# Kernel tuning notes

Measured on AMD Instinct MI355X. Metric: run time of the kernel, lower is better.

Reference implementation:

```python
import jax, jax.numpy as jnp
import numpy as np

# Hardcoded grouping buffer from GroupedPNMLP (6 groups x 4 nodes, permutation of 0..23)
GROUPING = np.array([[0, 3, 6, 9], [1, 4, 7, 10], [2, 5, 8, 11],
                     [12, 13, 14, 15], [16, 18, 20, 22], [17, 19, 21, 23]], dtype=np.int32)
INV_PERM = np.argsort(GROUPING.reshape(-1))  # scatter back to node order

N_SAMPLES = 131072
N_NODES = 24
IN_CH = 32
HID = 32
OUT_CH = 1
N_GROUPS = 6
NODES_PER_GROUP = 4


def setup_inputs() -> dict:
    key = jax.random.key(0)
    k = jax.random.split(key, 5)
    h = jax.random.normal(k[0], (N_SAMPLES, N_NODES, IN_CH), dtype=jnp.float32)
    valid = jax.random.randint(k[1], (N_SAMPLES, N_NODES), 0, 2).astype(jnp.int32)
    # Stacked ParallelLinear weights across the 6 group networks (D=2: in->W, W->out)
    W1 = jax.random.normal(k[2], (N_GROUPS, NODES_PER_GROUP, IN_CH, HID), dtype=jnp.float32) * 0.1
    b1 = jnp.zeros((N_GROUPS, NODES_PER_GROUP, HID), dtype=jnp.float32)
    W2 = jax.random.normal(k[3], (N_GROUPS, NODES_PER_GROUP, HID, OUT_CH), dtype=jnp.float32) * 0.1
    b2 = jnp.zeros((N_GROUPS, NODES_PER_GROUP, OUT_CH), dtype=jnp.float32)
    return {"h": h, "valid": valid, "W1": W1, "b1": b1, "W2": W2, "b2": b2}


def reference(h, valid, W1, b1, W2, b2):
    # Gather per-group node features: [N, 6, 4, 32]
    hg = h[:, GROUPING]
    # input_relu=True -> ReLU on input, then ParallelLinear -> ReLU -> ParallelLinear
    x = jnp.maximum(hg, 0.0)
    x = jnp.einsum('bgkl,gklj->bgkj', x, W1) + b1  # [N, 6, 4, 32]
    x = jnp.maximum(x, 0.0)
    out = jnp.einsum('bgkl,gklj->bgkj', x, W2) + b2  # [N, 6, 4, 1]
    # Samples whose group has no valid node are left as zeros (matches torch.where gather)
    group_valid = (valid[:, GROUPING].sum(-1) > 0)  # [N, 6]
    out = out * group_valid[:, :, None, None].astype(out.dtype)
    flat = out.reshape(out.shape[0], N_NODES, OUT_CH)
    # scatter_ with grouping indices == inverse permutation back to node order
    return flat[:, INV_PERM]
```

## Files before the change

kernel.cpp:

```cpp
#include <hip/hip_runtime.h>

#define N_NODES 24
#define CH 32

__global__ __launch_bounds__(256) void grouped_pnmlp_kernel(
    const float* __restrict__ h,
    const int*   __restrict__ valid,
    const float* __restrict__ W1,
    const float* __restrict__ b1,
    const float* __restrict__ W2,
    const float* __restrict__ b2,
    float*       __restrict__ out,
    int n_samples)
{
    const int node = blockIdx.y;

    int g, k;
    if (node < 12)      { g = node % 3;               k = node / 3;        }
    else if (node < 16) { g = 3;                      k = node - 12;       }
    else                { g = 4 + ((node - 16) & 1);  k = (node - 16) >> 1; }

    int vbase, vstride;
    if (g < 3)       { vbase = g;            vstride = 3; }
    else if (g == 3) { vbase = 12;           vstride = 1; }
    else             { vbase = 16 + (g - 4); vstride = 2; }

    const int gk = g * 4 + k;
    const float* __restrict__ w1  = W1 + (size_t)gk * CH * CH;
    const float* __restrict__ w2  = W2 + (size_t)gk * CH;
    const float* __restrict__ bb1 = b1 + (size_t)gk * CH;
    const float               bb2 = b2[gk];

    const int b = blockIdx.x * blockDim.x + threadIdx.x;
    if (b >= n_samples) return;

    const float4* __restrict__ xp =
        (const float4*)(h + ((size_t)b * N_NODES + node) * CH);
    float x[CH];
#pragma unroll
    for (int i = 0; i < 8; ++i) {
        float4 v = xp[i];
        x[4*i+0] = fmaxf(v.x, 0.0f);
        x[4*i+1] = fmaxf(v.y, 0.0f);
        x[4*i+2] = fmaxf(v.z, 0.0f);
        x[4*i+3] = fmaxf(v.w, 0.0f);
    }

    float hid[CH];
#pragma unroll
    for (int j = 0; j < CH; ++j) hid[j] = bb1[j];
#pragma unroll
    for (int l = 0; l < CH; ++l) {
        const float xl = x[l];
#pragma unroll
        for (int j = 0; j < CH; ++j)
            hid[j] = fmaf(xl, w1[l * CH + j], hid[j]);
    }

    float acc = bb2;
#pragma unroll
    for (int j = 0; j < CH; ++j)
        acc = fmaf(fmaxf(hid[j], 0.0f), w2[j], acc);

    const int* __restrict__ vrow = valid + (size_t)b * N_NODES;
    const int vs = vrow[vbase] + vrow[vbase + vstride] +
                   vrow[vbase + 2 * vstride] + vrow[vbase + 3 * vstride];

    out[(size_t)b * N_NODES + node] = (vs > 0) ? acc : 0.0f;
}

extern "C" void kernel_launch(void* const* d_in, const int* in_sizes, int n_in,
                              void* d_out, int out_size, void* d_ws, size_t ws_size,
                              hipStream_t stream) {
    const float* h     = (const float*)d_in[0];
    const int*   valid = (const int*)d_in[1];
    const float* W1    = (const float*)d_in[2];
    const float* b1    = (const float*)d_in[3];
    const float* W2    = (const float*)d_in[4];
    const float* b2    = (const float*)d_in[5];
    float* out = (float*)d_out;

    const int n_samples = in_sizes[0] / (N_NODES * CH);

    dim3 block(256, 1, 1);
    dim3 grid((n_samples + 255) / 256, N_NODES, 1);
    grouped_pnmlp_kernel<<<grid, block, 0, stream>>>(h, valid, W1, b1, W2, b2,
                                                     out, n_samples);
}
```

Baseline: 608.3 us.

## Stage contiguous node features in LDS with coalesced loads, one wave per node

Each block now covers 64 samples and 6 consecutive nodes. It loads the whole contiguous 6-node slab of h cooperatively as coalesced float4 reads into shared memory, applying the ReLU during the load. Each wave then handles one node, so the weight address is wave-uniform, and lanes read their sample's features from LDS instead of strided global loads. The validity masks are computed once per sample from vectorized int4 loads, and outputs are written out coalesced through shared memory. This adds two block barriers and about 50KB of LDS per block, which limits occupancy.

```diff
diff --git a/kernel.cpp b/kernel.cpp
--- a/kernel.cpp
+++ b/kernel.cpp
@@ -2,8 +2,11 @@
 
 #define N_NODES 24
 #define CH 32
+#define SPB 64
+#define NPQ 6
+#define THREADS 384
 
-__global__ __launch_bounds__(256) void grouped_pnmlp_kernel(
+__global__ __launch_bounds__(THREADS) void grouped_pnmlp_kernel(
     const float* __restrict__ h,
     const int*   __restrict__ valid,
     const float* __restrict__ W1,
@@ -13,17 +16,54 @@
     float*       __restrict__ out,
     int n_samples)
 {
-    const int node = blockIdx.y;
+    __shared__ float xs[SPB][196];
+    __shared__ float gs[SPB][6];
+    __shared__ float os[SPB][NPQ];
+
+    const int t  = threadIdx.x;
+    const int q  = blockIdx.y;
+    const int s0 = blockIdx.x * SPB;
+
+    const float4* __restrict__ hv = (const float4*)h;
+    float4 r[8];
+#pragma unroll
+    for (int i = 0; i < 8; ++i) {
+        const int f = i * THREADS + t;
+        const int s = f / 48, c = f % 48;
+        int sg = s0 + s; if (sg >= n_samples) sg = n_samples - 1;
+        r[i] = hv[(size_t)sg * 192 + q * 48 + c];
+    }
+#pragma unroll
+    for (int i = 0; i < 8; ++i) {
+        const int f = i * THREADS + t;
+        const int s = f / 48, c = f % 48;
+        float4 v = r[i];
+        v.x = fmaxf(v.x, 0.0f); v.y = fmaxf(v.y, 0.0f);
+        v.z = fmaxf(v.z, 0.0f); v.w = fmaxf(v.w, 0.0f);
+        *(float4*)&xs[s][4 * c] = v;
+    }
+
+    if (t < SPB) {
+        int sg = s0 + t; if (sg >= n_samples) sg = n_samples - 1;
+        const int4* __restrict__ vp = (const int4*)(valid + (size_t)sg * N_NODES);
+        const int4 a = vp[0], b = vp[1], c = vp[2], d = vp[3], e = vp[4], f = vp[5];
+        gs[t][0] = (a.x + a.w + b.z + c.y > 0) ? 1.0f : 0.0f;
+        gs[t][1] = (a.y + b.x + b.w + c.z > 0) ? 1.0f : 0.0f;
+        gs[t][2] = (a.z + b.y + c.x + c.w > 0) ? 1.0f : 0.0f;
+        gs[t][3] = (d.x + d.y + d.z + d.w > 0) ? 1.0f : 0.0f;
+        gs[t][4] = (e.x + e.z + f.x + f.z > 0) ? 1.0f : 0.0f;
+        gs[t][5] = (e.y + e.w + f.y + f.w > 0) ? 1.0f : 0.0f;
+    }
+    __syncthreads();
+
+    const int w    = __builtin_amdgcn_readfirstlane(t >> 6);
+    const int lane = t & 63;
+    const int node = q * NPQ + w;
 
     int g, k;
     if (node < 12)      { g = node % 3;               k = node / 3;        }
     else if (node < 16) { g = 3;                      k = node - 12;       }
     else                { g = 4 + ((node - 16) & 1);  k = (node - 16) >> 1; }
-
-    int vbase, vstride;
-    if (g < 3)       { vbase = g;            vstride = 3; }
-    else if (g == 3) { vbase = 12;           vstride = 1; }
-    else             { vbase = 16 + (g - 4); vstride = 2; }
 
     const int gk = g * 4 + k;
     const float* __restrict__ w1  = W1 + (size_t)gk * CH * CH;
@@ -31,19 +71,11 @@
     const float* __restrict__ bb1 = b1 + (size_t)gk * CH;
     const float               bb2 = b2[gk];
 
-    const int b = blockIdx.x * blockDim.x + threadIdx.x;
-    if (b >= n_samples) return;
-
-    const float4* __restrict__ xp =
-        (const float4*)(h + ((size_t)b * N_NODES + node) * CH);
     float x[CH];
 #pragma unroll
     for (int i = 0; i < 8; ++i) {
-        float4 v = xp[i];
-        x[4*i+0] = fmaxf(v.x, 0.0f);
-        x[4*i+1] = fmaxf(v.y, 0.0f);
-        x[4*i+2] = fmaxf(v.z, 0.0f);
-        x[4*i+3] = fmaxf(v.w, 0.0f);
+        const float4 v = *(const float4*)&xs[lane][w * CH + 4 * i];
+        x[4*i+0] = v.x; x[4*i+1] = v.y; x[4*i+2] = v.z; x[4*i+3] = v.w;
     }
 
     float hid[CH];
@@ -62,11 +94,15 @@
     for (int j = 0; j < CH; ++j)
         acc = fmaf(fmaxf(hid[j], 0.0f), w2[j], acc);
 
-    const int* __restrict__ vrow = valid + (size_t)b * N_NODES;
-    const int vs = vrow[vbase] + vrow[vbase + vstride] +
-                   vrow[vbase + 2 * vstride] + vrow[vbase + 3 * vstride];
+    os[lane][w] = acc * gs[lane][g];
+    __syncthreads();
 
-    out[(size_t)b * N_NODES + node] = (vs > 0) ? acc : 0.0f;
+    {
+        const int s = t / 6, j = t % 6;
+        const int sg = s0 + s;
+        if (sg < n_samples)
+            out[(size_t)sg * N_NODES + q * NPQ + j] = os[s][j];
+    }
 }
 
 extern "C" void kernel_launch(void* const* d_in, const int* in_sizes, int n_in,
@@ -82,8 +118,8 @@
 
     const int n_samples = in_sizes[0] / (N_NODES * CH);
 
-    dim3 block(256, 1, 1);
-    dim3 grid((n_samples + 255) / 256, N_NODES, 1);
+    dim3 block(THREADS, 1, 1);
+    dim3 grid((n_samples + SPB - 1) / SPB, 4, 1);
     grouped_pnmlp_kernel<<<grid, block, 0, stream>>>(h, valid, W1, b1, W2, b2,
                                                      out, n_samples);
 }
```

Measured after the change: 611.5 us. No clear change (+0.5%).

## Process 64 samples per block with waves looping over nodes and prefetching

Applied to the files above, without the earlier changes.

Replaces the per-node grid dimension with blocks of 64 samples, where each of 4 waves handles 6 nodes in turn, keeping the node index wave-uniform. The valid row is loaded once per sample as int4 vectors and all six group masks are computed up front, instead of four scalar loads per node. The next node's 128-byte feature row is prefetched into registers while the current node computes. This raises register pressure (cur and nxt buffers alongside the 32-wide hidden vector) and may lower occupancy. Weight reads stay wave-uniform, so they can still come from scalar loads.

```diff
diff --git a/kernel.cpp b/kernel.cpp
--- a/kernel.cpp
+++ b/kernel.cpp
@@ -2,8 +2,12 @@
 
 #define N_NODES 24
 #define CH 32
+#define SPW 64
+#define WAVES 4
+#define THREADS 256
+#define NPW 6
 
-__global__ __launch_bounds__(256) void grouped_pnmlp_kernel(
+__global__ __launch_bounds__(THREADS) void grouped_pnmlp_kernel(
     const float* __restrict__ h,
     const int*   __restrict__ valid,
     const float* __restrict__ W1,
@@ -13,60 +17,83 @@
     float*       __restrict__ out,
     int n_samples)
 {
-    const int node = blockIdx.y;
+    const int w    = __builtin_amdgcn_readfirstlane(threadIdx.x >> 6);
+    const int lane = threadIdx.x & 63;
 
-    int g, k;
-    if (node < 12)      { g = node % 3;               k = node / 3;        }
-    else if (node < 16) { g = 3;                      k = node - 12;       }
-    else                { g = 4 + ((node - 16) & 1);  k = (node - 16) >> 1; }
+    int s = blockIdx.x * SPW + lane;
+    const bool live = (s < n_samples);
+    if (!live) s = n_samples - 1;
 
-    int vbase, vstride;
-    if (g < 3)       { vbase = g;            vstride = 3; }
-    else if (g == 3) { vbase = 12;           vstride = 1; }
-    else             { vbase = 16 + (g - 4); vstride = 2; }
+    const int4* __restrict__ vp = (const int4*)(valid + (size_t)s * N_NODES);
+    const int4 a = vp[0], b = vp[1], c = vp[2], d = vp[3], e = vp[4], f = vp[5];
+    const float gv0 = (a.x + a.w + b.z + c.y > 0) ? 1.0f : 0.0f;
+    const float gv1 = (a.y + b.x + b.w + c.z > 0) ? 1.0f : 0.0f;
+    const float gv2 = (a.z + b.y + c.x + c.w > 0) ? 1.0f : 0.0f;
+    const float gv3 = (d.x + d.y + d.z + d.w > 0) ? 1.0f : 0.0f;
+    const float gv4 = (e.x + e.z + f.x + f.z > 0) ? 1.0f : 0.0f;
+    const float gv5 = (e.y + e.w + f.y + f.w > 0) ? 1.0f : 0.0f;
 
-    const int gk = g * 4 + k;
-    const float* __restrict__ w1  = W1 + (size_t)gk * CH * CH;
-    const float* __restrict__ w2  = W2 + (size_t)gk * CH;
-    const float* __restrict__ bb1 = b1 + (size_t)gk * CH;
-    const float               bb2 = b2[gk];
+    const float4* __restrict__ hrow = (const float4*)(h + (size_t)s * N_NODES * CH);
 
-    const int b = blockIdx.x * blockDim.x + threadIdx.x;
-    if (b >= n_samples) return;
+    float4 cur[8], nxt[8];
+#pragma unroll
+    for (int i = 0; i < 8; ++i) cur[i] = hrow[w * 8 + i];
 
-    const float4* __restrict__ xp =
-        (const float4*)(h + ((size_t)b * N_NODES + node) * CH);
-    float x[CH];
 #pragma unroll
-    for (int i = 0; i < 8; ++i) {
-        float4 v = xp[i];
-        x[4*i+0] = fmaxf(v.x, 0.0f);
-        x[4*i+1] = fmaxf(v.y, 0.0f);
-        x[4*i+2] = fmaxf(v.z, 0.0f);
-        x[4*i+3] = fmaxf(v.w, 0.0f);
-    }
+    for (int ni = 0; ni < NPW; ++ni) {
+        const int node = w + 4 * ni;
 
-    float hid[CH];
+        if (ni + 1 < NPW) {
 #pragma unroll
-    for (int j = 0; j < CH; ++j) hid[j] = bb1[j];
+            for (int i = 0; i < 8; ++i) nxt[i] = hrow[(node + 4) * 8 + i];
+        }
+
+        int g, k;
+        if (node < 12)      { g = node % 3;               k = node / 3;        }
+        else if (node < 16) { g = 3;                      k = node - 12;       }
+        else                { g = 4 + ((node - 16) & 1);  k = (node - 16) >> 1; }
+        const int gk = g * 4 + k;
+
+        const float* __restrict__ w1  = W1 + (size_t)gk * CH * CH;
+        const float* __restrict__ w2  = W2 + (size_t)gk * CH;
+        const float* __restrict__ bb1 = b1 + (size_t)gk * CH;
+        const float               bb2 = b2[gk];
+
+        float x[CH];
 #pragma unroll
-    for (int l = 0; l < CH; ++l) {
-        const float xl = x[l];
+        for (int i = 0; i < 8; ++i) {
+            x[4*i+0] = fmaxf(cur[i].x, 0.0f);
+            x[4*i+1] = fmaxf(cur[i].y, 0.0f);
+            x[4*i+2] = fmaxf(cur[i].z, 0.0f);
+            x[4*i+3] = fmaxf(cur[i].w, 0.0f);
+        }
+
+        float hid[CH];
+#pragma unroll
+        for (int j = 0; j < CH; ++j) hid[j] = bb1[j];
+#pragma unroll
+        for (int l = 0; l < CH; ++l) {
+            const float xl = x[l];
+#pragma unroll
+            for (int j = 0; j < CH; ++j)
+                hid[j] = fmaf(xl, w1[l * CH + j], hid[j]);
+        }
+
+        float acc = bb2;
 #pragma unroll
         for (int j = 0; j < CH; ++j)
-            hid[j] = fmaf(xl, w1[l * CH + j], hid[j]);
+            acc = fmaf(fmaxf(hid[j], 0.0f), w2[j], acc);
+
+        const float gvsel = (g == 0) ? gv0 : (g == 1) ? gv1 : (g == 2) ? gv2
+                          : (g == 3) ? gv3 : (g == 4) ? gv4 : gv5;
+
+        if (live) out[(size_t)s * N_NODES + node] = acc * gvsel;
+
+        if (ni + 1 < NPW) {
+#pragma unroll
+            for (int i = 0; i < 8; ++i) cur[i] = nxt[i];
+        }
     }
-
-    float acc = bb2;
-#pragma unroll
-    for (int j = 0; j < CH; ++j)
-        acc = fmaf(fmaxf(hid[j], 0.0f), w2[j], acc);
-
-    const int* __restrict__ vrow = valid + (size_t)b * N_NODES;
-    const int vs = vrow[vbase] + vrow[vbase + vstride] +
-                   vrow[vbase + 2 * vstride] + vrow[vbase + 3 * vstride];
-
-    out[(size_t)b * N_NODES + node] = (vs > 0) ? acc : 0.0f;
 }
 
 extern "C" void kernel_launch(void* const* d_in, const int* in_sizes, int n_in,
@@ -82,8 +109,8 @@
 
     const int n_samples = in_sizes[0] / (N_NODES * CH);
 
-    dim3 block(256, 1, 1);
-    dim3 grid((n_samples + 255) / 256, N_NODES, 1);
+    dim3 block(THREADS, 1, 1);
+    dim3 grid((n_samples + SPW - 1) / SPW, 1, 1);
     grouped_pnmlp_kernel<<<grid, block, 0, stream>>>(h, valid, W1, b1, W2, b2,
                                                      out, n_samples);
 }
```

Result: faster. 589.9 us (-3.0%).
